# Kernel tuning notes

Hardware: AMD Instinct MI355X
Metric: run time of the kernel (lower is better)

Reference implementation:

```python
import jax, jax.numpy as jnp
import numpy as np

N = 131072          # events
N_OBS = 64          # observables
HID = [512, 512, 512]          # trunk hidden widths
SUB_HID = [512, 256]           # per-pair subnetwork hidden widths
P = 3                          # number of pairings


def _glorot(key, shape):
    fan_in, fan_out = shape[-2], shape[-1]
    lim = np.sqrt(6.0 / (fan_in + fan_out)).astype(np.float32)
    return jax.random.uniform(key, shape, jnp.float32, -lim, lim)


def setup_inputs() -> dict:
    key = jax.random.key(0)
    ks = jax.random.split(key, 16)
    x = jax.random.normal(ks[0], (N, N_OBS), jnp.float32)
    y = jax.random.randint(ks[1], (N,), 0, 3)
    pairs = jnp.array([[0, 1], [0, 2], [1, 2]], dtype=jnp.int32)
    # trunk params
    W0 = _glorot(ks[2], (N_OBS, HID[0])); b0 = jnp.zeros((HID[0],), jnp.float32)
    W1 = _glorot(ks[3], (HID[0], HID[1])); b1 = jnp.zeros((HID[1],), jnp.float32)
    W2 = _glorot(ks[4], (HID[1], HID[2])); b2 = jnp.zeros((HID[2],), jnp.float32)
    # stacked per-pair subnetwork params (all P subnets share shapes)
    SW0 = _glorot(ks[5], (P, HID[2], SUB_HID[0])); Sb0 = jnp.zeros((P, SUB_HID[0]), jnp.float32)
    SW1 = _glorot(ks[6], (P, SUB_HID[0], SUB_HID[1])); Sb1 = jnp.zeros((P, SUB_HID[1]), jnp.float32)
    SW2 = _glorot(ks[7], (P, SUB_HID[1], 1)); Sb2 = jnp.zeros((P, 1), jnp.float32)
    return {"x": x, "y": y, "pairs": pairs,
            "W0": W0, "b0": b0, "W1": W1, "b1": b1, "W2": W2, "b2": b2,
            "SW0": SW0, "Sb0": Sb0, "SW1": SW1, "Sb1": Sb1, "SW2": SW2, "Sb2": Sb2}


def reference(x, y, pairs, W0, b0, W1, b1, W2, b2, SW0, Sb0, SW1, Sb1, SW2, Sb2):
    relu = jax.nn.relu
    # Trunk. Note: in the torch module with dropout_prob>0, the first Linear sits at
    # layer index 1, so the activation is applied to the raw input as well (eval-mode
    # dropout == identity). We reproduce that exactly.
    h = relu(x) @ W0 + b0
    h = relu(h) @ W1 + b1
    repr_ = relu(h) @ W2 + b2                      # [N, HID[-1]]

    # Per-pair membership masks (jit-safe stand-in for the variable-size gather):
    # mask[p, n] = True iff y[n] is one of the two labels of pairing p.
    mask = (y[None, :] == pairs[:, 0:1]) | (y[None, :] == pairs[:, 1:2])  # [P, N] bool

    # Per-pair RatioModel subnetworks, batched over the pair dim.
    # Same activation-before-every-Linear pattern as the trunk (dropout indices).
    hs = jnp.einsum('nd,pdh->pnh', relu(repr_), SW0) + Sb0[:, None, :]
    hs = jnp.einsum('pnh,phk->pnk', relu(hs), SW1) + Sb1[:, None, :]
    logit = jnp.einsum('pnk,pko->pno', relu(hs), SW2) + Sb2[:, None, :]  # [P, N, 1]
    s_hat = jnp.clip(jax.nn.sigmoid(logit[..., 0]), 1e-9, None)          # [P, N]
    r_hat = (1.0 - s_hat) / s_hat                                        # [P, N]

    maskf = mask.astype(s_hat.dtype)
    return repr_, r_hat * maskf, s_hat * maskf, mask
```

## Files before the change

### kernel.cpp

```cpp
#include <hip/hip_runtime.h>
#include <stdint.h>

#define NE 131072

typedef __attribute__((ext_vector_type(8))) short bf16x8;
typedef __attribute__((ext_vector_type(4))) float f32x4;

static __device__ __forceinline__ unsigned short f2bf(float f) {
  unsigned u = __float_as_uint(f);
  u += 0x7FFF + ((u >> 16) & 1);
  return (unsigned short)(u >> 16);
}
static __device__ __forceinline__ float bf2f(unsigned short h) {
  return __uint_as_float((unsigned)h << 16);
}
static __device__ __forceinline__ void gload_lds16(const void* g, void* l) {
  __builtin_amdgcn_global_load_lds(
      (const __attribute__((address_space(1))) unsigned*)g,
      (__attribute__((address_space(3))) unsigned*)l, 16, 0, 0);
}

__global__ void weight_prep(const float* __restrict__ W0, const float* __restrict__ W1,
                            const float* __restrict__ W2, const float* __restrict__ SW0,
                            const float* __restrict__ SW1, const float* __restrict__ SW2,
                            unsigned short* W0t, unsigned short* W1t,
                            unsigned short* W2t, unsigned short* SW0t,
                            unsigned short* SW1t, unsigned short* SW2b) {
  __shared__ float tile[32][33];
  const int u = blockIdx.y;
  const float* src; unsigned short* dst; int K, Nc;
  if (u == 0)      { src = W0;  dst = W0t;  K = 64;  Nc = 512; }
  else if (u == 1) { src = W1;  dst = W1t;  K = 512; Nc = 512; }
  else if (u == 2) { src = W2;  dst = W2t;  K = 512; Nc = 512; }
  else if (u < 6)  { int p = u - 3; src = SW0 + (long)p * 512 * 512; dst = SW0t + (long)p * 512 * 512; K = 512; Nc = 512; }
  else if (u < 9)  { int p = u - 6; src = SW1 + (long)p * 512 * 256; dst = SW1t + (long)p * 256 * 512; K = 512; Nc = 256; }
  else             { int p = u - 9; src = SW2 + (long)p * 256;       dst = SW2b + (long)p * 256;       K = 256; Nc = 1; }
  const int tkn = K >> 5;
  const int tk = blockIdx.x % tkn, tn = blockIdx.x / tkn;
  if (tn >= ((Nc + 31) >> 5)) return;
  const int k0 = tk * 32, n0 = tn * 32;
  const int tx = threadIdx.x & 31, ty = threadIdx.x >> 5;
  if (n0 + tx < Nc)
#pragma unroll
    for (int j = 0; j < 4; ++j)
      tile[ty * 4 + j][tx] = src[(long)(k0 + ty * 4 + j) * Nc + n0 + tx];
  __syncthreads();
#pragma unroll
  for (int j = 0; j < 4; ++j) {
    int n = n0 + ty * 4 + j;
    if (n < Nc) dst[(long)n * K + k0 + tx] = f2bf(tile[tx][ty * 4 + j]);
  }
}

__global__ void relu_cvt_x(const float4* __restrict__ x,
                           ushort4* __restrict__ xb) {
  int i = blockIdx.x * blockDim.x + threadIdx.x;
  float4 v = x[i];
  ushort4 o;
  o.x = f2bf(fmaxf(v.x, 0.f));
  o.y = f2bf(fmaxf(v.y, 0.f));
  o.z = f2bf(fmaxf(v.z, 0.f));
  o.w = f2bf(fmaxf(v.w, 0.f));
  xb[i] = o;
}

__global__ void build_idx(const int* __restrict__ y, const int* __restrict__ pairs,
                          int chunkRows, int* __restrict__ idxL,
                          int* __restrict__ posA, int* __restrict__ cnts) {
  const int c = blockIdx.x, p = blockIdx.y;
  const int la = pairs[p * 2], lb = pairs[p * 2 + 1];
  const long r0 = (long)c * chunkRows;
  const long cb = r0;
  __shared__ int wbase[4];
  __shared__ int running;
  if (threadIdx.x == 0) running = 0;
  __syncthreads();
  const int lane = threadIdx.x & 63, wv = threadIdx.x >> 6;
  for (int it = 0; it < chunkRows / 256; ++it) {
    const int r = it * 256 + threadIdx.x;
    const int yv = y[r0 + r];
    const bool act = (yv == la) || (yv == lb);
    const unsigned long long m = __ballot(act);
    const int rank = __popcll(m & ((1ull << lane) - 1));
    if (lane == 0) wbase[wv] = __popcll(m);
    __syncthreads();
    int wb = 0;
#pragma unroll
    for (int w = 0; w < 4; ++w) wb += (w < wv) ? wbase[w] : 0;
    const int tot = wbase[0] + wbase[1] + wbase[2] + wbase[3];
    if (act) {
      const int posi = running + wb + rank;
      idxL[(long)p * NE + cb + posi] = r;
      posA[(long)p * NE + r0 + r] = (int)(cb + posi);
    } else {
      posA[(long)p * NE + r0 + r] = -1;
    }
    __syncthreads();
    if (threadIdx.x == 0) running += tot;
    __syncthreads();
  }
  const int cnt = running;
  if (threadIdx.x == 0) cnts[c * 3 + p] = cnt;
  const int padded = (cnt + 255) & ~255;
  const int last = (cnt > 0) ? idxL[(long)p * NE + cb + cnt - 1] : 0;
  for (int i = cnt + threadIdx.x; i < padded; i += 256)
    idxL[(long)p * NE + cb + i] = last;
}

__global__ __launch_bounds__(512, 4) void gemmT(
    const unsigned short* __restrict__ A, long aZ,
    const unsigned short* __restrict__ Bt, long bZ,
    const float* __restrict__ bias, long biasZ,
    float* __restrict__ outF,
    unsigned short* __restrict__ outA, long cZ,
    int K, int Nc,
    const unsigned short* __restrict__ w2, long w2Z,
    float* __restrict__ PB, long pbZ, int r0,
    const int* __restrict__ aIdx, long aIdxZ,
    const int* __restrict__ cnts) {
  __shared__ unsigned short lds[3 * 12288];
  __shared__ float part[4][128];
  const int z = blockIdx.z;
  const long brow = (long)blockIdx.x * 128;
  if (cnts) {
    const int cp = cnts[z];
    if ((int)brow >= ((cp + 255) & ~255)) return;
  }
  A += (long)z * aZ;
  Bt += (long)z * bZ;
  bias += (long)z * biasZ;
  if (outA) outA += (long)z * cZ;
  if (w2) { w2 += (long)z * w2Z; PB += (long)z * pbZ; }
  if (aIdx) aIdx += (long)z * aIdxZ;

  const int tid = threadIdx.x, wave = tid >> 6, lane = tid & 63;
  const int wm = wave >> 2, wn = wave & 3;
  const int lr = lane & 15, lh = lane >> 4;
  const int bcol = blockIdx.y * 256;
  const int nk = K >> 5;
  const int axr = (lh ^ ((lr >> 1) & 3)) * 8;

  const int arL = tid >> 2;
  const int arow = aIdx ? aIdx[brow + arL] : (int)(brow + arL);

  f32x4 acc[4][4];
#pragma unroll
  for (int m = 0; m < 4; ++m)
#pragma unroll
    for (int n = 0; n < 4; ++n) acc[m][n] = (f32x4){0.f, 0.f, 0.f, 0.f};

  auto STAGE = [&](int t) {
    if (t >= nk) return;
    unsigned short* dst = &lds[(t % 3) * 12288];
    const int k0 = t << 5;
    {
      const int c = tid;
      const int r = c >> 2;
      const int kc = (c & 3) ^ ((r >> 1) & 3);
      gload_lds16(A + (long)arow * K + k0 + kc * 8, &dst[(wave * 64) * 8]);
    }
#pragma unroll
    for (int i = 0; i < 2; ++i) {
      const int cb = i * 512 + wave * 64;
      const int c = cb + lane;
      const int r = c >> 2;
      const int kc = (c & 3) ^ ((r >> 1) & 3);
      gload_lds16(Bt + (long)(bcol + r) * K + k0 + kc * 8,
                  &dst[(512 + cb) * 8]);
    }
  };

  STAGE(0);
  STAGE(1);

  for (int t = 0; t < nk; ++t) {
    if (t < nk - 1)
      asm volatile("s_waitcnt vmcnt(3)" ::: "memory");
    else
      asm volatile("s_waitcnt vmcnt(0)" ::: "memory");
    __builtin_amdgcn_s_barrier();
    __builtin_amdgcn_sched_barrier(0);
    const unsigned short* buf = &lds[(t % 3) * 12288];
    bf16x8 a[4], b[4];
#pragma unroll
    for (int m = 0; m < 4; ++m)
      a[m] = *(const bf16x8*)&buf[(wm * 64 + m * 16 + lr) * 32 + axr];
#pragma unroll
    for (int n = 0; n < 4; ++n)
      b[n] = *(const bf16x8*)&buf[512 * 8 + (wn * 64 + n * 16 + lr) * 32 + axr];
    STAGE(t + 2);
    __builtin_amdgcn_s_setprio(1);
#pragma unroll
    for (int m = 0; m < 4; ++m)
#pragma unroll
      for (int n = 0; n < 4; ++n)
        acc[m][n] =
            __builtin_amdgcn_mfma_f32_16x16x32_bf16(a[m], b[n], acc[m][n], 0, 0, 0);
    __builtin_amdgcn_s_setprio(0);
  }

  float bv[4];
#pragma unroll
  for (int n = 0; n < 4; ++n) bv[n] = bias[bcol + wn * 64 + n * 16 + lr];

  if (!w2) {
#pragma unroll
    for (int m = 0; m < 4; ++m) {
#pragma unroll
      for (int r = 0; r < 4; ++r) {
        long e = brow + wm * 64 + m * 16 + lh * 4 + r;
#pragma unroll
        for (int n = 0; n < 4; ++n) {
          int oc = bcol + wn * 64 + n * 16 + lr;
          float v = acc[m][n][r] + bv[n];
          if (outF) outF[e * Nc + oc] = v;
          if (outA) outA[e * Nc + oc] = f2bf(fmaxf(v, 0.f));
        }
      }
    }
  } else {
    float w2v[4];
#pragma unroll
    for (int n = 0; n < 4; ++n) w2v[n] = bf2f(w2[wn * 64 + n * 16 + lr]);
#pragma unroll
    for (int m = 0; m < 4; ++m) {
#pragma unroll
      for (int r = 0; r < 4; ++r) {
        float s = 0.f;
#pragma unroll
        for (int n = 0; n < 4; ++n)
          s += fmaxf(acc[m][n][r] + bv[n], 0.f) * w2v[n];
#pragma unroll
        for (int off = 1; off < 16; off <<= 1) s += __shfl_xor(s, off);
        if (lr == 0) part[wn][wm * 64 + m * 16 + lh * 4 + r] = s;
      }
    }
    __syncthreads();
    if (tid < 128)
      PB[r0 + brow + tid] =
          part[0][tid] + part[1][tid] + part[2][tid] + part[3][tid];
  }
}

__global__ void head_final(const float* __restrict__ PB,
                           const int* __restrict__ posA,
                           const float* __restrict__ Sb2,
                           float* __restrict__ outR, float* __restrict__ outS,
                           float* __restrict__ outM) {
  const long n = (long)blockIdx.x * 256 + threadIdx.x;
  const int p = blockIdx.y;
  const int pos = posA[(long)p * NE + n];
  float rr = 0.f, s = 0.f, mf = 0.f;
  if (pos >= 0) {
    float logit = PB[(long)p * NE + pos] + Sb2[p];
    s = 1.f / (1.f + expf(-logit));
    s = fmaxf(s, 1e-9f);
    rr = (1.f - s) / s;
    mf = 1.f;
  }
  outR[(long)p * NE + n] = rr;
  outS[(long)p * NE + n] = s;
  outM[(long)p * NE + n] = mf;
}

extern "C" void kernel_launch(void* const* d_in, const int* in_sizes, int n_in,
                              void* d_out, int out_size, void* d_ws, size_t ws_size,
                              hipStream_t stream) {
  const float* x   = (const float*)d_in[0];
  const int*   y   = (const int*)d_in[1];
  const int*   prs = (const int*)d_in[2];
  const float* W0  = (const float*)d_in[3];
  const float* b0  = (const float*)d_in[4];
  const float* W1  = (const float*)d_in[5];
  const float* b1  = (const float*)d_in[6];
  const float* W2  = (const float*)d_in[7];
  const float* b2  = (const float*)d_in[8];
  const float* SW0 = (const float*)d_in[9];
  const float* Sb0 = (const float*)d_in[10];
  const float* SW1 = (const float*)d_in[11];
  const float* Sb1 = (const float*)d_in[12];
  const float* SW2 = (const float*)d_in[13];
  const float* Sb2 = (const float*)d_in[14];

  uint8_t* ws = (uint8_t*)d_ws;
  size_t off = 0;
  auto take = [&](size_t bytes) -> void* {
    void* ptr = ws + off;
    off = (off + bytes + 255) & ~(size_t)255;
    return ptr;
  };
  unsigned short* W0t  = (unsigned short*)take((size_t)64 * 512 * 2);
  unsigned short* W1t  = (unsigned short*)take((size_t)512 * 512 * 2);
  unsigned short* W2t  = (unsigned short*)take((size_t)512 * 512 * 2);
  unsigned short* SW0t = (unsigned short*)take((size_t)3 * 512 * 512 * 2);
  unsigned short* SW1t = (unsigned short*)take((size_t)3 * 256 * 512 * 2);
  unsigned short* SW2b = (unsigned short*)take((size_t)3 * 256 * 2);
  unsigned short* Xb   = (unsigned short*)take((size_t)NE * 64 * 2);
  float*          PB   = (float*)take((size_t)3 * NE * 4);
  int*            idxL = (int*)take((size_t)3 * NE * 4);
  int*            posA = (int*)take((size_t)3 * NE * 4);
  int*            cnts = (int*)take((size_t)64 * 4);
  const size_t fixed = off;

  long chunk = 65536;
  while (chunk > 8192 && fixed + (size_t)6 * chunk * 1024 + 4096 > ws_size)
    chunk >>= 1;
  const int nchunks = (int)(NE / chunk);

  unsigned short* T0   = (unsigned short*)take((size_t)chunk * 512 * 2);
  unsigned short* T1   = (unsigned short*)take((size_t)chunk * 512 * 2);
  unsigned short* bufR = (unsigned short*)take((size_t)chunk * 512 * 2);
  unsigned short* H3   = (unsigned short*)take((size_t)3 * chunk * 512 * 2);

  float* out   = (float*)d_out;
  float* outRe = out;
  float* outR  = out + (size_t)NE * 512;
  float* outS  = outR + (size_t)3 * NE;
  float* outM  = outS + (size_t)3 * NE;

  weight_prep<<<dim3(256, 12), 256, 0, stream>>>(W0, W1, W2, SW0, SW1, SW2,
                                                 W0t, W1t, W2t, SW0t, SW1t, SW2b);
  relu_cvt_x<<<dim3(NE * 64 / 4 / 256), 256, 0, stream>>>((const float4*)x,
                                                          (ushort4*)Xb);
  build_idx<<<dim3(nchunks, 3), 256, 0, stream>>>(y, prs, (int)chunk,
                                                  idxL, posA, cnts);

  for (int c = 0; c < nchunks; ++c) {
    const long r0 = (long)c * chunk;
    gemmT<<<dim3(chunk / 128, 2, 1), 512, 0, stream>>>(
        Xb + r0 * 64, 0, W0t, 0, b0, 0, nullptr, T0, 0, 64, 512,
        nullptr, 0, nullptr, 0, 0, nullptr, 0, nullptr);
    gemmT<<<dim3(chunk / 128, 2, 1), 512, 0, stream>>>(
        T0, 0, W1t, 0, b1, 0, nullptr, T1, 0, 512, 512,
        nullptr, 0, nullptr, 0, 0, nullptr, 0, nullptr);
    gemmT<<<dim3(chunk / 128, 2, 1), 512, 0, stream>>>(
        T1, 0, W2t, 0, b2, 0, outRe + r0 * 512, bufR, 0, 512, 512,
        nullptr, 0, nullptr, 0, 0, nullptr, 0, nullptr);
    gemmT<<<dim3(chunk / 128, 2, 3), 512, 0, stream>>>(
        bufR, 0, SW0t, (long)512 * 512, Sb0, 512, nullptr,
        H3, (long)chunk * 512, 512, 512,
        nullptr, 0, nullptr, 0, 0, idxL + r0, NE, cnts + c * 3);
    gemmT<<<dim3(chunk / 128, 1, 3), 512, 0, stream>>>(
        H3, (long)chunk * 512, SW1t, (long)256 * 512, Sb1, 256, nullptr,
        nullptr, 0, 512, 256,
        SW2b, 256, PB, (long)NE, (int)r0, nullptr, 0, cnts + c * 3);
  }
  head_final<<<dim3(NE / 256, 3), 256, 0, stream>>>(PB, posA, Sb2,
                                                    outR, outS, outM);
}
```

Measured before the change: 754.3 us.

## Decouple trunk and subnet chunk sizes, storing full trunk output buffer

Splits the single chunk loop into two: the trunk GEMMs run over a large chunk and write the bf16 representation for all events into a full-size buffer, then the per-pair subnetwork GEMMs run over smaller fixed 32K-event chunks. The aim is to keep the per-pair intermediate H3 smaller, likely so it stays cache-resident, while the trunk keeps large launches. In exchange it needs a full N×512 bf16 workspace buffer and issues more subnet launches.

```diff
diff --git a/kernel.cpp b/kernel.cpp
--- a/kernel.cpp
+++ b/kernel.cpp
@@ -2,6 +2,7 @@
 #include <stdint.h>
 
 #define NE 131072
+#define SBCH 32768
 
 typedef __attribute__((ext_vector_type(8))) short bf16x8;
 typedef __attribute__((ext_vector_type(4))) float f32x4;
@@ -302,15 +303,16 @@
   int*            cnts = (int*)take((size_t)64 * 4);
   const size_t fixed = off;
 
-  long chunk = 65536;
-  while (chunk > 8192 && fixed + (size_t)6 * chunk * 1024 + 4096 > ws_size)
-    chunk >>= 1;
-  const int nchunks = (int)(NE / chunk);
-
-  unsigned short* T0   = (unsigned short*)take((size_t)chunk * 512 * 2);
-  unsigned short* T1   = (unsigned short*)take((size_t)chunk * 512 * 2);
-  unsigned short* bufR = (unsigned short*)take((size_t)chunk * 512 * 2);
-  unsigned short* H3   = (unsigned short*)take((size_t)3 * chunk * 512 * 2);
+  long trch = 65536;
+  while (trch > SBCH &&
+         fixed + (size_t)2 * trch * 1024 + (size_t)NE * 1024 +
+                 (size_t)3 * SBCH * 1024 + 4096 > ws_size)
+    trch >>= 1;
+
+  unsigned short* T0   = (unsigned short*)take((size_t)trch * 512 * 2);
+  unsigned short* T1   = (unsigned short*)take((size_t)trch * 512 * 2);
+  unsigned short* bufR = (unsigned short*)take((size_t)NE * 512 * 2);
+  unsigned short* H3   = (unsigned short*)take((size_t)3 * SBCH * 512 * 2);
 
   float* out   = (float*)d_out;
   float* outRe = out;
@@ -322,26 +324,29 @@
                                                  W0t, W1t, W2t, SW0t, SW1t, SW2b);
   relu_cvt_x<<<dim3(NE * 64 / 4 / 256), 256, 0, stream>>>((const float4*)x,
                                                           (ushort4*)Xb);
-  build_idx<<<dim3(nchunks, 3), 256, 0, stream>>>(y, prs, (int)chunk,
-                                                  idxL, posA, cnts);
-
-  for (int c = 0; c < nchunks; ++c) {
-    const long r0 = (long)c * chunk;
-    gemmT<<<dim3(chunk / 128, 2, 1), 512, 0, stream>>>(
+  build_idx<<<dim3(NE / SBCH, 3), 256, 0, stream>>>(y, prs, SBCH,
+                                                    idxL, posA, cnts);
+
+  for (long r0 = 0; r0 < NE; r0 += trch) {
+    gemmT<<<dim3(trch / 128, 2, 1), 512, 0, stream>>>(
         Xb + r0 * 64, 0, W0t, 0, b0, 0, nullptr, T0, 0, 64, 512,
         nullptr, 0, nullptr, 0, 0, nullptr, 0, nullptr);
-    gemmT<<<dim3(chunk / 128, 2, 1), 512, 0, stream>>>(
+    gemmT<<<dim3(trch / 128, 2, 1), 512, 0, stream>>>(
         T0, 0, W1t, 0, b1, 0, nullptr, T1, 0, 512, 512,
         nullptr, 0, nullptr, 0, 0, nullptr, 0, nullptr);
-    gemmT<<<dim3(chunk / 128, 2, 1), 512, 0, stream>>>(
-        T1, 0, W2t, 0, b2, 0, outRe + r0 * 512, bufR, 0, 512, 512,
+    gemmT<<<dim3(trch / 128, 2, 1), 512, 0, stream>>>(
+        T1, 0, W2t, 0, b2, 0, outRe + r0 * 512, bufR + r0 * 512, 0, 512, 512,
         nullptr, 0, nullptr, 0, 0, nullptr, 0, nullptr);
-    gemmT<<<dim3(chunk / 128, 2, 3), 512, 0, stream>>>(
-        bufR, 0, SW0t, (long)512 * 512, Sb0, 512, nullptr,
-        H3, (long)chunk * 512, 512, 512,
+  }
+
+  for (int c = 0; c < NE / SBCH; ++c) {
+    const long r0 = (long)c * SBCH;
+    gemmT<<<dim3(SBCH / 128, 2, 3), 512, 0, stream>>>(
+        bufR + r0 * 512, 0, SW0t, (long)512 * 512, Sb0, 512, nullptr,
+        H3, (long)SBCH * 512, 512, 512,
         nullptr, 0, nullptr, 0, 0, idxL + r0, NE, cnts + c * 3);
-    gemmT<<<dim3(chunk / 128, 1, 3), 512, 0, stream>>>(
-        H3, (long)chunk * 512, SW1t, (long)256 * 512, Sb1, 256, nullptr,
+    gemmT<<<dim3(SBCH / 128, 1, 3), 512, 0, stream>>>(
+        H3, (long)SBCH * 512, SW1t, (long)256 * 512, Sb1, 256, nullptr,
         nullptr, 0, 512, 256,
         SW2b, 256, PB, (long)NE, (int)r0, nullptr, 0, cnts + c * 3);
   }
```

After: 722.3 us. 1.04x faster.
